# Performance work log

Measured on AMD Instinct MI355X. Metric: run time of the kernel, lower is better.

## Reference

```python
import jax, jax.numpy as jnp
import numpy as np

N_NODES = 50000
N_EDGES = 600000
DIM = 128
NUM_CLASSES = 10
EPS = 1e-15
MAX_NORM = 1.0 - 1e-5  # keep points strictly inside the unit ball for artanh


def _norm(x):
    return jnp.maximum(jnp.linalg.norm(x, axis=-1, keepdims=True), EPS)


def logmap0(x):
    # Poincare ball, c=1: artanh(||x||) * x / ||x||
    n = _norm(x)
    return jnp.arctanh(jnp.minimum(n, MAX_NORM)) * x / n


def expmap0(u):
    # Poincare ball, c=1: tanh(||u||) * u / ||u||
    n = _norm(u)
    return jnp.tanh(n) * u / n


def hyp_conv(x, W, b, src, dst):
    t = logmap0(x)                       # [N, D] manifold -> tangent at origin
    h = t @ W.T + b                      # [N, D] linear in tangent space
    y = expmap0(h)                       # [N, D] back to manifold
    # message passing: gather source features, scatter-add at destinations
    return jax.ops.segment_sum(y[src], dst, num_segments=N_NODES)


def setup_inputs() -> dict:
    key = jax.random.key(0)
    ks = jax.random.split(key, 8)
    edge_index = jax.random.randint(ks[0], (2, N_EDGES), 0, N_NODES, dtype=jnp.int64)
    # entity embeddings: small tangent vectors mapped onto the ball
    x = expmap0(0.01 * jax.random.normal(ks[1], (N_NODES, DIM), dtype=jnp.float32))
    s = 1.0 / np.sqrt(DIM)
    W1 = jax.random.normal(ks[2], (DIM, DIM), dtype=jnp.float32) * s
    b1 = jax.random.normal(ks[3], (DIM,), dtype=jnp.float32) * 0.01
    W2 = jax.random.normal(ks[4], (DIM, DIM), dtype=jnp.float32) * s
    b2 = jax.random.normal(ks[5], (DIM,), dtype=jnp.float32) * 0.01
    Wc = jax.random.normal(ks[6], (NUM_CLASSES, DIM), dtype=jnp.float32) * s
    bc = jax.random.normal(ks[7], (NUM_CLASSES,), dtype=jnp.float32) * 0.01
    return {"edge_index": edge_index, "x": x, "W1": W1, "b1": b1,
            "W2": W2, "b2": b2, "Wc": Wc, "bc": bc}


def reference(edge_index, x, W1, b1, W2, b2, Wc, bc):
    src, dst = edge_index[0], edge_index[1]
    h = hyp_conv(x, W1, b1, src, dst)
    h = jax.nn.relu(h)
    h = hyp_conv(h, W2, b2, src, dst)
    h = jax.nn.relu(h)
    t = logmap0(h)
    return t @ Wc.T + bc  # [N_NODES, NUM_CLASSES]
```

## Files before the change

### kernel.cpp

```cpp
#include <hip/hip_runtime.h>

#define N_NODES 50000
#define N_EDGES 600000
#define DIM 128
#define NCLS 10
#define ELLW 64
#define CURSTRIDE 16
#define EPSF 1e-15f
#define MAXNORM 0.99999f
#define NTILE ((N_NODES + 63) / 64)
#define FILLB 586
#define XFB 512

typedef __attribute__((ext_vector_type(8))) short bf16x8;
typedef __attribute__((ext_vector_type(4))) float f32x4;

__device__ inline float waveSum(float v) {
#pragma unroll
  for (int o = 1; o < 64; o <<= 1) v += __shfl_xor(v, o, 64);
  return v;
}

__device__ inline unsigned short f2bf(float f) {
  union { float f; unsigned u; } c; c.f = f;
  return (unsigned short)((c.u + 0x7FFFu + ((c.u >> 16) & 1u)) >> 16);
}
__device__ inline float bf_lo(unsigned u) {
  union { unsigned u; float f; } c; c.u = u << 16; return c.f;
}
__device__ inline float bf_hi(unsigned u) {
  union { unsigned u; float f; } c; c.u = u & 0xFFFF0000u; return c.f;
}

__global__ __launch_bounds__(256) void init_kernel(
    int* __restrict__ cursor, const float* __restrict__ W1, const float* __restrict__ W2,
    unsigned short* __restrict__ W1b, unsigned short* __restrict__ W2b)
{
  int i = blockIdx.x * 256 + threadIdx.x;
  if (i < N_NODES) cursor[i * CURSTRIDE] = 0;
  if (i < DIM * DIM) {
    W1b[i] = f2bf(W1[i]);
    W2b[i] = f2bf(W2[i]);
  }
}

__global__ __launch_bounds__(256, 2) void fill_transform(
    const int* __restrict__ src, const int* __restrict__ dst,
    int* __restrict__ cursor, int* __restrict__ ell,
    const float* __restrict__ x, const unsigned short* __restrict__ Wb,
    const float* __restrict__ b, unsigned short* __restrict__ y)
{
  __shared__ __align__(16) unsigned short At[64 * DIM];

  if (blockIdx.x < FILLB) {
    const int nthr = FILLB * 256;
    const int e = blockIdx.x * 256 + threadIdx.x;
    const int e0 = e, e1 = e + nthr, e2 = e + 2 * nthr, e3 = e + 3 * nthr;
    int d0, d1, d2, d3, s0, s1, s2, s3;
    if (e0 < N_EDGES) { d0 = dst[e0]; s0 = src[e0]; }
    if (e1 < N_EDGES) { d1 = dst[e1]; s1 = src[e1]; }
    if (e2 < N_EDGES) { d2 = dst[e2]; s2 = src[e2]; }
    if (e3 < N_EDGES) { d3 = dst[e3]; s3 = src[e3]; }
    int p0, p1, p2, p3;
    if (e0 < N_EDGES) p0 = atomicAdd(&cursor[d0 * CURSTRIDE], 1);
    if (e1 < N_EDGES) p1 = atomicAdd(&cursor[d1 * CURSTRIDE], 1);
    if (e2 < N_EDGES) p2 = atomicAdd(&cursor[d2 * CURSTRIDE], 1);
    if (e3 < N_EDGES) p3 = atomicAdd(&cursor[d3 * CURSTRIDE], 1);
    if (e0 < N_EDGES) ell[d0 * ELLW + p0] = s0;
    if (e1 < N_EDGES) ell[d1 * ELLW + p1] = s1;
    if (e2 < N_EDGES) ell[d2 * ELLW + p2] = s2;
    if (e3 < N_EDGES) ell[d3 * ELLW + p3] = s3;
    return;
  }

  const int tid = threadIdx.x;
  const int w = tid >> 6;
  const int l = tid & 63;
  const int lr = l & 15;
  const int lg = l >> 4;

  bf16x8 bf[8][4];
#pragma unroll
  for (int n = 0; n < 8; ++n)
#pragma unroll
    for (int kc = 0; kc < 4; ++kc)
      bf[n][kc] = *(const bf16x8*)(Wb + (n * 16 + lr) * DIM + kc * 32 + lg * 8);

  float bias[8];
#pragma unroll
  for (int n = 0; n < 8; ++n) bias[n] = b[n * 16 + lr];

  const int row = w * 16 + lr;

  for (int tile = blockIdx.x - FILLB; tile < NTILE; tile += XFB) {
    const int base = tile * 64;
    const int node = base + row;
    __syncthreads();

    float v[32];
    if (node < N_NODES) {
      const float4* xr = (const float4*)(x + (size_t)node * DIM + lg * 32);
#pragma unroll
      for (int q = 0; q < 8; ++q) {
        float4 f = xr[q];
        v[q * 4 + 0] = f.x; v[q * 4 + 1] = f.y; v[q * 4 + 2] = f.z; v[q * 4 + 3] = f.w;
      }
    } else {
#pragma unroll
      for (int q = 0; q < 32; ++q) v[q] = 0.f;
    }
    float sq = 0.f;
#pragma unroll
    for (int q = 0; q < 32; ++q) sq += v[q] * v[q];
    sq += __shfl_xor(sq, 16, 64);
    sq += __shfl_xor(sq, 32, 64);
    float n1 = sqrtf(sq);
    float nc = fmaxf(n1, EPSF);
    float nm = fminf(nc, MAXNORM);
    float scale = 0.5f * logf((1.f + nm) / (1.f - nm)) / nc;
#pragma unroll
    for (int s = 0; s < 4; ++s) {
      unsigned short tmp[8];
#pragma unroll
      for (int e = 0; e < 8; ++e) tmp[e] = f2bf(v[s * 8 + e] * scale);
      int byte = row * 256 + lg * 64 + s * 16;
      byte ^= (row & 7) << 4;
      *(bf16x8*)((char*)At + byte) = *(const bf16x8*)tmp;
    }
    __syncthreads();

    f32x4 acc[8];
#pragma unroll
    for (int n = 0; n < 8; ++n) {
      acc[n][0] = bias[n]; acc[n][1] = bias[n]; acc[n][2] = bias[n]; acc[n][3] = bias[n];
    }
#pragma unroll
    for (int kc = 0; kc < 4; ++kc) {
      int byte = row * 256 + kc * 64 + lg * 16;
      byte ^= (row & 7) << 4;
      bf16x8 af = *(const bf16x8*)((const char*)At + byte);
#pragma unroll
      for (int n = 0; n < 8; ++n)
        acc[n] = __builtin_amdgcn_mfma_f32_16x16x32_bf16(af, bf[n][kc], acc[n], 0, 0, 0);
    }

    float rs[4];
#pragma unroll
    for (int j = 0; j < 4; ++j) {
      float s2 = 0.f;
#pragma unroll
      for (int n = 0; n < 8; ++n) s2 += acc[n][j] * acc[n][j];
      s2 += __shfl_xor(s2, 1, 64);
      s2 += __shfl_xor(s2, 2, 64);
      s2 += __shfl_xor(s2, 4, 64);
      s2 += __shfl_xor(s2, 8, 64);
      float n2 = sqrtf(s2);
      float n2c = fmaxf(n2, EPSF);
      rs[j] = tanhf(n2c) / n2c;
    }
#pragma unroll
    for (int j = 0; j < 4; ++j) {
      int nrow = base + w * 16 + lg * 4 + j;
      if (nrow < N_NODES) {
        unsigned short* yr = y + (size_t)nrow * DIM + lr;
#pragma unroll
        for (int n = 0; n < 8; ++n) yr[n * 16] = f2bf(acc[n][j] * rs[j]);
      }
    }
  }
}

__global__ __launch_bounds__(256) void gatherT_kernel(
    const unsigned short* __restrict__ y, const int* __restrict__ cursor,
    const int* __restrict__ ell, unsigned short* __restrict__ tout)
{
  const int node = blockIdx.x * 4 + (threadIdx.x >> 6);
  if (node >= N_NODES) return;
  const int lane = threadIdx.x & 63;
  const int cnt = cursor[node * CURSTRIDE];
  const int* lst = ell + (size_t)node * ELLW;
  const int myidx = (lane < cnt) ? lst[lane] : 0;

  float2 a0 = {0.f, 0.f}, a1 = {0.f, 0.f}, a2 = {0.f, 0.f}, a3 = {0.f, 0.f};
  int j = 0;
  for (; j + 7 < cnt; j += 8) {
    int s0 = __shfl(myidx, j    , 64);
    int s1 = __shfl(myidx, j + 1, 64);
    int s2 = __shfl(myidx, j + 2, 64);
    int s3 = __shfl(myidx, j + 3, 64);
    int s4 = __shfl(myidx, j + 4, 64);
    int s5 = __shfl(myidx, j + 5, 64);
    int s6 = __shfl(myidx, j + 6, 64);
    int s7 = __shfl(myidx, j + 7, 64);
    unsigned u0 = ((const unsigned*)(y + (size_t)s0 * DIM))[lane];
    unsigned u1 = ((const unsigned*)(y + (size_t)s1 * DIM))[lane];
    unsigned u2 = ((const unsigned*)(y + (size_t)s2 * DIM))[lane];
    unsigned u3 = ((const unsigned*)(y + (size_t)s3 * DIM))[lane];
    unsigned u4 = ((const unsigned*)(y + (size_t)s4 * DIM))[lane];
    unsigned u5 = ((const unsigned*)(y + (size_t)s5 * DIM))[lane];
    unsigned u6 = ((const unsigned*)(y + (size_t)s6 * DIM))[lane];
    unsigned u7 = ((const unsigned*)(y + (size_t)s7 * DIM))[lane];
    a0.x += bf_lo(u0); a0.y += bf_hi(u0);
    a1.x += bf_lo(u1); a1.y += bf_hi(u1);
    a2.x += bf_lo(u2); a2.y += bf_hi(u2);
    a3.x += bf_lo(u3); a3.y += bf_hi(u3);
    a0.x += bf_lo(u4); a0.y += bf_hi(u4);
    a1.x += bf_lo(u5); a1.y += bf_hi(u5);
    a2.x += bf_lo(u6); a2.y += bf_hi(u6);
    a3.x += bf_lo(u7); a3.y += bf_hi(u7);
  }
  for (; j + 3 < cnt; j += 4) {
    int s0 = __shfl(myidx, j    , 64);
    int s1 = __shfl(myidx, j + 1, 64);
    int s2 = __shfl(myidx, j + 2, 64);
    int s3 = __shfl(myidx, j + 3, 64);
    unsigned u0 = ((const unsigned*)(y + (size_t)s0 * DIM))[lane];
    unsigned u1 = ((const unsigned*)(y + (size_t)s1 * DIM))[lane];
    unsigned u2 = ((const unsigned*)(y + (size_t)s2 * DIM))[lane];
    unsigned u3 = ((const unsigned*)(y + (size_t)s3 * DIM))[lane];
    a0.x += bf_lo(u0); a0.y += bf_hi(u0);
    a1.x += bf_lo(u1); a1.y += bf_hi(u1);
    a2.x += bf_lo(u2); a2.y += bf_hi(u2);
    a3.x += bf_lo(u3); a3.y += bf_hi(u3);
  }
  for (; j < cnt; ++j) {
    int s0 = __shfl(myidx, j, 64);
    unsigned u0 = ((const unsigned*)(y + (size_t)s0 * DIM))[lane];
    a0.x += bf_lo(u0); a0.y += bf_hi(u0);
  }
  float2 r;
  r.x = fmaxf((a0.x + a1.x) + (a2.x + a3.x), 0.f);
  r.y = fmaxf((a0.y + a1.y) + (a2.y + a3.y), 0.f);

  float s = waveSum(r.x * r.x + r.y * r.y);
  float n = sqrtf(s);
  float nc = fmaxf(n, EPSF);
  float nm = fminf(nc, MAXNORM);
  float scale = 0.5f * logf((1.0f + nm) / (1.0f - nm)) / nc;
  unsigned u = (unsigned)f2bf(r.x * scale) | ((unsigned)f2bf(r.y * scale) << 16);
  ((unsigned*)(tout + (size_t)node * DIM))[lane] = u;
}

__global__ __launch_bounds__(256, 2) void transform2_mfma(
    const unsigned short* __restrict__ t, const unsigned short* __restrict__ Wb,
    const float* __restrict__ b, unsigned short* __restrict__ y)
{
  const int tid = threadIdx.x;
  const int w = tid >> 6;
  const int l = tid & 63;
  const int lr = l & 15;
  const int lg = l >> 4;

  __shared__ __align__(16) unsigned short At[64 * DIM];

  bf16x8 bf[8][4];
#pragma unroll
  for (int n = 0; n < 8; ++n)
#pragma unroll
    for (int kc = 0; kc < 4; ++kc)
      bf[n][kc] = *(const bf16x8*)(Wb + (n * 16 + lr) * DIM + kc * 32 + lg * 8);

  float bias[8];
#pragma unroll
  for (int n = 0; n < 8; ++n) bias[n] = b[n * 16 + lr];

  const int row = w * 16 + lr;

  for (int tile = blockIdx.x; tile < NTILE; tile += gridDim.x) {
    const int base = tile * 64;
    const int node = base + row;
    __syncthreads();

#pragma unroll
    for (int s = 0; s < 4; ++s) {
      bf16x8 frag;
      if (node < N_NODES)
        frag = *(const bf16x8*)(t + (size_t)node * DIM + lg * 32 + s * 8);
      else
        frag = bf16x8{0, 0, 0, 0, 0, 0, 0, 0};
      int byte = row * 256 + lg * 64 + s * 16;
      byte ^= (row & 7) << 4;
      *(bf16x8*)((char*)At + byte) = frag;
    }
    __syncthreads();

    f32x4 acc[8];
#pragma unroll
    for (int n = 0; n < 8; ++n) {
      acc[n][0] = bias[n]; acc[n][1] = bias[n]; acc[n][2] = bias[n]; acc[n][3] = bias[n];
    }
#pragma unroll
    for (int kc = 0; kc < 4; ++kc) {
      int byte = row * 256 + kc * 64 + lg * 16;
      byte ^= (row & 7) << 4;
      bf16x8 af = *(const bf16x8*)((const char*)At + byte);
#pragma unroll
      for (int n = 0; n < 8; ++n)
        acc[n] = __builtin_amdgcn_mfma_f32_16x16x32_bf16(af, bf[n][kc], acc[n], 0, 0, 0);
    }

    float rs[4];
#pragma unroll
    for (int j = 0; j < 4; ++j) {
      float s2 = 0.f;
#pragma unroll
      for (int n = 0; n < 8; ++n) s2 += acc[n][j] * acc[n][j];
      s2 += __shfl_xor(s2, 1, 64);
      s2 += __shfl_xor(s2, 2, 64);
      s2 += __shfl_xor(s2, 4, 64);
      s2 += __shfl_xor(s2, 8, 64);
      float n2 = sqrtf(s2);
      float n2c = fmaxf(n2, EPSF);
      rs[j] = tanhf(n2c) / n2c;
    }
#pragma unroll
    for (int j = 0; j < 4; ++j) {
      int nrow = base + w * 16 + lg * 4 + j;
      if (nrow < N_NODES) {
        unsigned short* yr = y + (size_t)nrow * DIM + lr;
#pragma unroll
        for (int n = 0; n < 8; ++n) yr[n * 16] = f2bf(acc[n][j] * rs[j]);
      }
    }
  }
}

__global__ __launch_bounds__(256) void head_mfma(
    const unsigned short* __restrict__ t2, const float* __restrict__ Wc,
    const float* __restrict__ bc, float* __restrict__ out)
{
  const int base = blockIdx.x * 64;
  const int w = threadIdx.x >> 6;
  const int l = threadIdx.x & 63;
  const int lr = l & 15;
  const int lg = l >> 4;

  bf16x8 bw[4];
#pragma unroll
  for (int kc = 0; kc < 4; ++kc) {
    unsigned short tmp[8];
    if (lr < NCLS) {
      const float* wr = Wc + (size_t)lr * DIM + kc * 32 + lg * 8;
#pragma unroll
      for (int e = 0; e < 8; ++e) tmp[e] = f2bf(wr[e]);
    } else {
#pragma unroll
      for (int e = 0; e < 8; ++e) tmp[e] = 0;
    }
    bw[kc] = *(const bf16x8*)tmp;
  }
  const float bias = (lr < NCLS) ? bc[lr] : 0.f;

  const int arow = base + w * 16 + lr;
  f32x4 acc;
  acc[0] = bias; acc[1] = bias; acc[2] = bias; acc[3] = bias;
#pragma unroll
  for (int kc = 0; kc < 4; ++kc) {
    bf16x8 af;
    if (arow < N_NODES)
      af = *(const bf16x8*)(t2 + (size_t)arow * DIM + kc * 32 + lg * 8);
    else
      af = bf16x8{0, 0, 0, 0, 0, 0, 0, 0};
    acc = __builtin_amdgcn_mfma_f32_16x16x32_bf16(af, bw[kc], acc, 0, 0, 0);
  }

  if (lr < NCLS) {
#pragma unroll
    for (int j = 0; j < 4; ++j) {
      int nrow = base + w * 16 + lg * 4 + j;
      if (nrow < N_NODES) out[(size_t)nrow * NCLS + lr] = acc[j];
    }
  }
}

extern "C" void kernel_launch(void* const* d_in, const int* in_sizes, int n_in,
                              void* d_out, int out_size, void* d_ws, size_t ws_size,
                              hipStream_t stream)
{
  const int* edge = (const int*)d_in[0];
  const int* src = edge;
  const int* dst = edge + N_EDGES;
  const float* x  = (const float*)d_in[1];
  const float* W1 = (const float*)d_in[2];
  const float* b1 = (const float*)d_in[3];
  const float* W2 = (const float*)d_in[4];
  const float* b2 = (const float*)d_in[5];
  const float* Wc = (const float*)d_in[6];
  const float* bc = (const float*)d_in[7];
  float* out = (float*)d_out;

  unsigned short* ybuf = (unsigned short*)d_ws;
  unsigned short* tbuf = ybuf + (size_t)N_NODES * DIM;
  unsigned short* W1b = tbuf + (size_t)N_NODES * DIM;
  unsigned short* W2b = W1b + DIM * DIM;
  int* cursor = (int*)(W2b + DIM * DIM);
  int* ell = cursor + (size_t)N_NODES * CURSTRIDE;

  init_kernel<<<(N_NODES + 255) / 256, 256, 0, stream>>>(cursor, W1, W2, W1b, W2b);

  fill_transform<<<FILLB + XFB, 256, 0, stream>>>(src, dst, cursor, ell, x, W1b, b1, ybuf);

  gatherT_kernel<<<(N_NODES + 3) / 4, 256, 0, stream>>>(ybuf, cursor, ell, tbuf);

  transform2_mfma<<<512, 256, 0, stream>>>(tbuf, W2b, b2, ybuf);

  gatherT_kernel<<<(N_NODES + 3) / 4, 256, 0, stream>>>(ybuf, cursor, ell, tbuf);

  head_mfma<<<NTILE, 256, 0, stream>>>(tbuf, Wc, bc, out);
}
```

Measured before the change: 130.9 us.

## Store ELL indices as 16-bit and issue sixteen masked gather loads up front

Neighbor lists in the ELL buffer are stored as unsigned short instead of int, which halves the index traffic written by the fill pass and read by the gather. This relies on node IDs staying below 65536. The gather kernel now always issues 16 row loads at once and masks out entries past the node's degree, then handles any remaining neighbors in chunks of 8. With an average degree around 12, most nodes finish in one batch of independent loads rather than a chain of count-dependent loops, at the cost of some redundant loads of row 0.

```diff
diff --git a/kernel.cpp b/kernel.cpp
--- a/kernel.cpp
+++ b/kernel.cpp
@@ -46,7 +46,7 @@
 
 __global__ __launch_bounds__(256, 2) void fill_transform(
     const int* __restrict__ src, const int* __restrict__ dst,
-    int* __restrict__ cursor, int* __restrict__ ell,
+    int* __restrict__ cursor, unsigned short* __restrict__ ell,
     const float* __restrict__ x, const unsigned short* __restrict__ Wb,
     const float* __restrict__ b, unsigned short* __restrict__ y)
 {
@@ -66,10 +66,10 @@
     if (e1 < N_EDGES) p1 = atomicAdd(&cursor[d1 * CURSTRIDE], 1);
     if (e2 < N_EDGES) p2 = atomicAdd(&cursor[d2 * CURSTRIDE], 1);
     if (e3 < N_EDGES) p3 = atomicAdd(&cursor[d3 * CURSTRIDE], 1);
-    if (e0 < N_EDGES) ell[d0 * ELLW + p0] = s0;
-    if (e1 < N_EDGES) ell[d1 * ELLW + p1] = s1;
-    if (e2 < N_EDGES) ell[d2 * ELLW + p2] = s2;
-    if (e3 < N_EDGES) ell[d3 * ELLW + p3] = s3;
+    if (e0 < N_EDGES) ell[(size_t)d0 * ELLW + p0] = (unsigned short)s0;
+    if (e1 < N_EDGES) ell[(size_t)d1 * ELLW + p1] = (unsigned short)s1;
+    if (e2 < N_EDGES) ell[(size_t)d2 * ELLW + p2] = (unsigned short)s2;
+    if (e3 < N_EDGES) ell[(size_t)d3 * ELLW + p3] = (unsigned short)s3;
     return;
   }
 
@@ -172,62 +172,49 @@
 
 __global__ __launch_bounds__(256) void gatherT_kernel(
     const unsigned short* __restrict__ y, const int* __restrict__ cursor,
-    const int* __restrict__ ell, unsigned short* __restrict__ tout)
+    const unsigned short* __restrict__ ell, unsigned short* __restrict__ tout)
 {
   const int node = blockIdx.x * 4 + (threadIdx.x >> 6);
   if (node >= N_NODES) return;
   const int lane = threadIdx.x & 63;
   const int cnt = cursor[node * CURSTRIDE];
-  const int* lst = ell + (size_t)node * ELLW;
-  const int myidx = (lane < cnt) ? lst[lane] : 0;
+  const unsigned short* lst = ell + (size_t)node * ELLW;
+  const int myidx = (lane < cnt) ? (int)lst[lane] : 0;
 
   float2 a0 = {0.f, 0.f}, a1 = {0.f, 0.f}, a2 = {0.f, 0.f}, a3 = {0.f, 0.f};
-  int j = 0;
-  for (; j + 7 < cnt; j += 8) {
-    int s0 = __shfl(myidx, j    , 64);
-    int s1 = __shfl(myidx, j + 1, 64);
-    int s2 = __shfl(myidx, j + 2, 64);
-    int s3 = __shfl(myidx, j + 3, 64);
-    int s4 = __shfl(myidx, j + 4, 64);
-    int s5 = __shfl(myidx, j + 5, 64);
-    int s6 = __shfl(myidx, j + 6, 64);
-    int s7 = __shfl(myidx, j + 7, 64);
-    unsigned u0 = ((const unsigned*)(y + (size_t)s0 * DIM))[lane];
-    unsigned u1 = ((const unsigned*)(y + (size_t)s1 * DIM))[lane];
-    unsigned u2 = ((const unsigned*)(y + (size_t)s2 * DIM))[lane];
-    unsigned u3 = ((const unsigned*)(y + (size_t)s3 * DIM))[lane];
-    unsigned u4 = ((const unsigned*)(y + (size_t)s4 * DIM))[lane];
-    unsigned u5 = ((const unsigned*)(y + (size_t)s5 * DIM))[lane];
-    unsigned u6 = ((const unsigned*)(y + (size_t)s6 * DIM))[lane];
-    unsigned u7 = ((const unsigned*)(y + (size_t)s7 * DIM))[lane];
-    a0.x += bf_lo(u0); a0.y += bf_hi(u0);
-    a1.x += bf_lo(u1); a1.y += bf_hi(u1);
-    a2.x += bf_lo(u2); a2.y += bf_hi(u2);
-    a3.x += bf_lo(u3); a3.y += bf_hi(u3);
-    a0.x += bf_lo(u4); a0.y += bf_hi(u4);
-    a1.x += bf_lo(u5); a1.y += bf_hi(u5);
-    a2.x += bf_lo(u6); a2.y += bf_hi(u6);
-    a3.x += bf_lo(u7); a3.y += bf_hi(u7);
-  }
-  for (; j + 3 < cnt; j += 4) {
-    int s0 = __shfl(myidx, j    , 64);
-    int s1 = __shfl(myidx, j + 1, 64);
-    int s2 = __shfl(myidx, j + 2, 64);
-    int s3 = __shfl(myidx, j + 3, 64);
-    unsigned u0 = ((const unsigned*)(y + (size_t)s0 * DIM))[lane];
-    unsigned u1 = ((const unsigned*)(y + (size_t)s1 * DIM))[lane];
-    unsigned u2 = ((const unsigned*)(y + (size_t)s2 * DIM))[lane];
-    unsigned u3 = ((const unsigned*)(y + (size_t)s3 * DIM))[lane];
-    a0.x += bf_lo(u0); a0.y += bf_hi(u0);
-    a1.x += bf_lo(u1); a1.y += bf_hi(u1);
-    a2.x += bf_lo(u2); a2.y += bf_hi(u2);
-    a3.x += bf_lo(u3); a3.y += bf_hi(u3);
-  }
-  for (; j < cnt; ++j) {
-    int s0 = __shfl(myidx, j, 64);
-    unsigned u0 = ((const unsigned*)(y + (size_t)s0 * DIM))[lane];
-    a0.x += bf_lo(u0); a0.y += bf_hi(u0);
-  }
+
+  unsigned uu[16];
+#pragma unroll
+  for (int q = 0; q < 16; ++q) {
+    int sidx = __shfl(myidx, q, 64);
+    uu[q] = ((const unsigned*)(y + (size_t)sidx * DIM))[lane];
+  }
+#pragma unroll
+  for (int q = 0; q < 16; ++q) {
+    float vx = (q < cnt) ? bf_lo(uu[q]) : 0.f;
+    float vy = (q < cnt) ? bf_hi(uu[q]) : 0.f;
+    switch (q & 3) {
+      case 0: a0.x += vx; a0.y += vy; break;
+      case 1: a1.x += vx; a1.y += vy; break;
+      case 2: a2.x += vx; a2.y += vy; break;
+      default: a3.x += vx; a3.y += vy; break;
+    }
+  }
+  for (int j = 16; j < cnt; j += 8) {
+    unsigned ut[8];
+#pragma unroll
+    for (int q = 0; q < 8; ++q) {
+      int sidx = __shfl(myidx, j + q, 64);
+      ut[q] = ((const unsigned*)(y + (size_t)sidx * DIM))[lane];
+    }
+#pragma unroll
+    for (int q = 0; q < 8; ++q) {
+      float vx = (j + q < cnt) ? bf_lo(ut[q]) : 0.f;
+      float vy = (j + q < cnt) ? bf_hi(ut[q]) : 0.f;
+      a0.x += vx; a0.y += vy;
+    }
+  }
+
   float2 r;
   r.x = fmaxf((a0.x + a1.x) + (a2.x + a3.x), 0.f);
   r.y = fmaxf((a0.y + a1.y) + (a2.y + a3.y), 0.f);
@@ -393,8 +380,8 @@
   unsigned short* tbuf = ybuf + (size_t)N_NODES * DIM;
   unsigned short* W1b = tbuf + (size_t)N_NODES * DIM;
   unsigned short* W2b = W1b + DIM * DIM;
-  int* cursor = (int*)(W2b + DIM * DIM);
-  int* ell = cursor + (size_t)N_NODES * CURSTRIDE;
+  unsigned short* ell = W2b + DIM * DIM;
+  int* cursor = (int*)(ell + (size_t)N_NODES * ELLW);
 
   init_kernel<<<(N_NODES + 255) / 256, 256, 0, stream>>>(cursor, W1, W2, W1b, W2b);
 
```

Result: faster. 127.7 us (-2.4%).
